# Performance work log

Measured on AMD Instinct MI355X. Metric: run time of the kernel, lower is better.

## Reference

```python
import jax, jax.numpy as jnp
import numpy as np

B, NMAX, D, H = 8, 8192, 256, 8
DH = D // H  # 32
EPS = 1e-5


def _ln(x, g, b):
    mu = jnp.mean(x, axis=-1, keepdims=True)
    var = jnp.mean((x - mu) ** 2, axis=-1, keepdims=True)
    return (x - mu) / jnp.sqrt(var + EPS) * g + b


def setup_inputs() -> dict:
    key = jax.random.key(0)
    ks = jax.random.split(key, 14)
    s = 1.0 / np.sqrt(D)

    def lin(k):
        kw, kb = jax.random.split(k)
        W = jax.random.uniform(kw, (D, D), minval=-s, maxval=s, dtype=jnp.float32)
        b = jax.random.uniform(kb, (D,), minval=-s, maxval=s, dtype=jnp.float32)
        return W, b

    Wh, bh = lin(ks[0])
    Wq, bq = lin(ks[1])
    Wk, bk = lin(ks[2])
    Wv, bv = lin(ks[3])
    Wout, bout = lin(ks[4])
    return {
        "x": jax.random.normal(ks[5], (B * NMAX, D), dtype=jnp.float32),
        "node_prob": jax.random.uniform(ks[6], (B, NMAX), dtype=jnp.float32),
        "Wh": Wh, "bh": bh,
        "Wq": Wq, "bq": bq,
        "Wk": Wk, "bk": bk,
        "Wv": Wv, "bv": bv,
        "Wout": Wout, "bout": bout,
        "ln1_g": jnp.ones((D,), jnp.float32), "ln1_b": jnp.zeros((D,), jnp.float32),
        "ln2_g": jnp.ones((D,), jnp.float32), "ln2_b": jnp.zeros((D,), jnp.float32),
        "beta_b": jnp.full((D,), 0.5, jnp.float32),  # self.b with beta=0.5 >= 0
    }


def reference(x, node_prob, Wh, bh, Wq, bq, Wk, bk, Wv, bv, Wout, bout,
              ln1_g, ln1_b, ln2_g, ln2_b, beta_b):
    x0 = _ln(x, ln1_g, ln1_b)          # [N, D] input_norm
    h = x0 @ Wh + bh                   # [N, D]
    xd = x0.reshape(B, NMAX, D)        # to_dense_batch (equal-size graphs)
    k = jax.nn.sigmoid(xd @ Wk + bk)   # [B, Nmax, D]
    q = jax.nn.sigmoid(xd @ Wq + bq)   # qk_shared=False
    v = xd @ Wv + bv
    k = k * node_prob[:, :, None]      # node-prob weighting
    q = q.reshape(B, NMAX, H, DH)
    k = k.reshape(B, NMAX, H, DH)
    v = v.reshape(B, NMAX, H, DH)
    kv = jnp.einsum('bnhd,bnhe->bhde', k, v)        # k^T v per head
    num = jnp.einsum('bnhd,bhde->bnhe', q, kv)      # q . kv
    den = jnp.einsum('bnhd,bhd->bnh', q, jnp.sum(k, axis=1))[..., None]
    att = (num / den).reshape(B * NMAX, D)
    out = _ln(att, ln2_g, ln2_b) * (h + beta_b)     # norm(x) * (h + beta)
    out = jax.nn.relu(out @ Wout + bout)            # dropout p=0 / eval: identity
    return out + x0                                  # residual=True
```

## Files before the change

kernel.cpp:

```cpp
#include <hip/hip_runtime.h>
#include <cstdint>


#define DEVI __device__ __forceinline__

typedef __attribute__((ext_vector_type(8))) short bf16x8;
typedef __attribute__((ext_vector_type(4))) float f32x4;

DEVI ushort f2bf(float f) {
  uint32_t u = __float_as_uint(f);
  u += 0x7FFFu + ((u >> 16) & 1u);
  return (ushort)(u >> 16);
}
DEVI float bf2f(ushort h) { return __uint_as_float(((uint32_t)h) << 16); }

DEVI void gload_lds16(const void* g, void* l) {
  __builtin_amdgcn_global_load_lds((const __attribute__((address_space(1))) void*)g,
                                   (__attribute__((address_space(3))) void*)l, 16, 0, 0);
}
DEVI void vm_drain() { asm volatile("s_waitcnt vmcnt(0)" ::: "memory"); }

__global__ __launch_bounds__(256)
void ln1_k(const float* __restrict__ x, const float* __restrict__ g1,
           const float* __restrict__ b1, ushort* __restrict__ x0b,
           const float* __restrict__ Wh, const float* __restrict__ Wq,
           const float* __restrict__ Wk, const float* __restrict__ Wv,
           const float* __restrict__ Wout,
           const float* __restrict__ bh, const float* __restrict__ bq,
           const float* __restrict__ bk, const float* __restrict__ bv,
           ushort* __restrict__ Wcat_t, ushort* __restrict__ Woutt,
           float* __restrict__ bcat, float* __restrict__ kv, float* __restrict__ ksum)
{
  const int t = threadIdx.x;
  const int idx = blockIdx.x * 256 + t;
  if (idx < 396288) {
    if (idx < 262144) {
      int j = idx >> 8, kk = idx & 255;
      int g = j >> 8, jj = j & 255;
      const float* W = (g == 0) ? Wh : (g == 1) ? Wq : (g == 2) ? Wk : Wv;
      Wcat_t[idx] = f2bf(W[kk * 256 + jj]);
    }
    int i2 = idx - 262144;
    if (i2 >= 0 && i2 < 65536) {
      int j = i2 >> 8, kk = i2 & 255;
      Woutt[i2] = f2bf(Wout[kk * 256 + j]);
    }
    int i3 = idx - (262144 + 65536);
    if (i3 >= 0 && i3 < 1024) {
      int g = i3 >> 8, jj = i3 & 255;
      const float* bb = (g == 0) ? bh : (g == 1) ? bq : (g == 2) ? bk : bv;
      bcat[i3] = bb[jj];
    }
    int i4 = idx - (262144 + 65536 + 1024);
    if (i4 >= 0 && i4 < 65536) kv[i4] = 0.0f;
    int i5 = idx - (262144 + 65536 + 1024 + 65536);
    if (i5 >= 0 && i5 < 2048) ksum[i5] = 0.0f;
  }
  const int l = t & 63, w = t >> 6;
  const size_t r = (size_t)blockIdx.x * 4 + w;
  const float4 xv = *(const float4*)&x[r * 256 + l * 4];
  float s = xv.x + xv.y + xv.z + xv.w;
  float sq = xv.x * xv.x + xv.y * xv.y + xv.z * xv.z + xv.w * xv.w;
#pragma unroll
  for (int off = 1; off < 64; off <<= 1) { s += __shfl_xor(s, off); sq += __shfl_xor(sq, off); }
  const float mean = s * (1.0f / 256.0f);
  const float var = sq * (1.0f / 256.0f) - mean * mean;
  const float rstd = rsqrtf(var + 1e-5f);
  const float4 g4 = *(const float4*)&g1[l * 4];
  const float4 b4 = *(const float4*)&b1[l * 4];
  ushort4 o;
  o.x = f2bf((xv.x - mean) * rstd * g4.x + b4.x);
  o.y = f2bf((xv.y - mean) * rstd * g4.y + b4.y);
  o.z = f2bf((xv.z - mean) * rstd * g4.z + b4.z);
  o.w = f2bf((xv.w - mean) * rstd * g4.w + b4.w);
  *(ushort4*)&x0b[r * 256 + l * 4] = o;
}

template <int MODE>
__global__ __launch_bounds__(256, 4)
void gemm_bf16_k(const ushort* __restrict__ A, const ushort* __restrict__ Bt,
                 const float* __restrict__ bias, const float* __restrict__ node_prob,
                 const ushort* __restrict__ x0b, ushort* __restrict__ outb,
                 float* __restrict__ outf)
{
  __shared__ ushort smem[16384];
  const int t = threadIdx.x;
  const int l = t & 63;
  const int w = t >> 6;
  const int wr = w >> 1, wc = w & 1;
  const int nNB = (MODE == 0) ? 8 : 2;
  const int per = gridDim.x >> 3;
  const int tile = (blockIdx.x & 7) * per + (blockIdx.x >> 3);
  const int m0 = (tile / nNB) * 128, n0 = (tile % nNB) * 128;
  const int sr = t >> 2;
  const int sd = t & 3;
  const int ssl = sd ^ ((t >> 3) & 3);
  f32x4 acc[4][4] = {};

  auto stage = [&](int buf, int kt) {
#pragma unroll
    for (int i = 0; i < 2; ++i) {
      int row = i * 64 + sr;
      gload_lds16(&A[(size_t)(m0 + row) * 256 + kt * 32 + ssl * 8],
                  &smem[buf * 4096 + row * 32 + sd * 8]);
    }
#pragma unroll
    for (int i = 0; i < 2; ++i) {
      int row = i * 64 + sr;
      gload_lds16(&Bt[(size_t)(n0 + row) * 256 + kt * 32 + ssl * 8],
                  &smem[8192 + buf * 4096 + row * 32 + sd * 8]);
    }
  };

  stage(0, 0);
  vm_drain();
  __syncthreads();
  const int fr = l & 15;
  const int fq = l >> 4;
  const int fsl = (fq ^ ((l >> 1) & 3)) * 8;
#pragma unroll
  for (int kt = 0; kt < 8; ++kt) {
    const int cur = kt & 1;
    if (kt < 7) stage(cur ^ 1, kt + 1);
    bf16x8 af[4], bfr[4];
#pragma unroll
    for (int f = 0; f < 4; ++f) {
      af[f]  = *(const bf16x8*)&smem[cur * 4096 + (wr * 64 + f * 16 + fr) * 32 + fsl];
      bfr[f] = *(const bf16x8*)&smem[8192 + cur * 4096 + (wc * 64 + f * 16 + fr) * 32 + fsl];
    }
#pragma unroll
    for (int fm = 0; fm < 4; ++fm)
#pragma unroll
      for (int fn = 0; fn < 4; ++fn)
        acc[fm][fn] = __builtin_amdgcn_mfma_f32_16x16x32_bf16(af[fm], bfr[fn], acc[fm][fn], 0, 0, 0);
    vm_drain();
    __syncthreads();
  }

  float biasv[4];
#pragma unroll
  for (int fn = 0; fn < 4; ++fn) biasv[fn] = bias[n0 + wc * 64 + fn * 16 + fr];
  const int g = n0 >> 8;
#pragma unroll
  for (int fm = 0; fm < 4; ++fm) {
#pragma unroll
    for (int fn = 0; fn < 4; ++fn) {
#pragma unroll
      for (int i = 0; i < 4; ++i) {
        const int row = wr * 64 + fm * 16 + fq * 4 + i;
        const int col = wc * 64 + fn * 16 + fr;
        float v = acc[fm][fn][i] + biasv[fn];
        if (MODE == 0) {
          if (g == 1 || g == 2) v = 1.0f / (1.0f + __expf(-v));
          if (g == 2) v *= node_prob[m0 + row];
        } else {
          v = fmaxf(v, 0.0f);
        }
        smem[row * 128 + (col ^ ((row & 7) << 4))] = f2bf(v);
      }
    }
  }
  __syncthreads();
#pragma unroll
  for (int it = 0; it < 8; ++it) {
    const int row = w * 32 + it * 4 + fq;
    const int c8 = fr * 8;
    bf16x8 u = *(const bf16x8*)&smem[row * 128 + (c8 ^ ((row & 7) << 4))];
    if (MODE == 0) {
      *(bf16x8*)&outb[(size_t)(m0 + row) * 1024 + n0 + c8] = u;
    } else {
      bf16x8 xv = *(const bf16x8*)&x0b[(size_t)(m0 + row) * 256 + n0 + c8];
      float4 o0, o1;
      o0.x = bf2f((ushort)u[0]) + bf2f((ushort)xv[0]);
      o0.y = bf2f((ushort)u[1]) + bf2f((ushort)xv[1]);
      o0.z = bf2f((ushort)u[2]) + bf2f((ushort)xv[2]);
      o0.w = bf2f((ushort)u[3]) + bf2f((ushort)xv[3]);
      o1.x = bf2f((ushort)u[4]) + bf2f((ushort)xv[4]);
      o1.y = bf2f((ushort)u[5]) + bf2f((ushort)xv[5]);
      o1.z = bf2f((ushort)u[6]) + bf2f((ushort)xv[6]);
      o1.w = bf2f((ushort)u[7]) + bf2f((ushort)xv[7]);
      *(float4*)&outf[(size_t)(m0 + row) * 256 + n0 + c8] = o0;
      *(float4*)&outf[(size_t)(m0 + row) * 256 + n0 + c8 + 4] = o1;
    }
  }
}

__global__ __launch_bounds__(256)
void kvred_k(const ushort* __restrict__ hqkv, float* __restrict__ kv, float* __restrict__ ksum)
{
  __shared__ ushort smem[32768];
  const int t = threadIdx.x, l = t & 63, w = t >> 6;
  const int bh = blockIdx.x >> 4, cb = blockIdx.x & 15;
  const int b = bh >> 3, h = bh & 7;
  const size_t nbase = (size_t)b * 8192 + cb * 512 + w * 128;
  ushort* kt = &smem[w * 8192];
  ushort* vt = &smem[w * 8192 + 4096];
#pragma unroll
  for (int i = 0; i < 8; ++i) {
    size_t row = nbase + i * 16 + (l >> 2);
    gload_lds16(&hqkv[row * 1024 + 512 + h * 32 + (l & 3) * 8], &kt[i * 512 + l * 8]);
  }
#pragma unroll
  for (int i = 0; i < 8; ++i) {
    size_t row = nbase + i * 16 + (l >> 2);
    gload_lds16(&hqkv[row * 1024 + 768 + h * 32 + (l & 3) * 8], &vt[i * 512 + l * 8]);
  }
  vm_drain();

  const int d0 = (l & 7) * 4, e0 = (l >> 3) * 4;
  float acc[4][4] = {};
  float ks0 = 0, ks1 = 0, ks2 = 0, ks3 = 0;
#pragma unroll 8
  for (int nn = 0; nn < 128; ++nn) {
    ushort4 kk = *(const ushort4*)&kt[nn * 32 + d0];
    ushort4 vv = *(const ushort4*)&vt[nn * 32 + e0];
    float k0 = bf2f(kk.x), k1 = bf2f(kk.y), k2 = bf2f(kk.z), k3 = bf2f(kk.w);
    float v0 = bf2f(vv.x), v1 = bf2f(vv.y), v2 = bf2f(vv.z), v3 = bf2f(vv.w);
    acc[0][0] += k0 * v0; acc[0][1] += k0 * v1; acc[0][2] += k0 * v2; acc[0][3] += k0 * v3;
    acc[1][0] += k1 * v0; acc[1][1] += k1 * v1; acc[1][2] += k1 * v2; acc[1][3] += k1 * v3;
    acc[2][0] += k2 * v0; acc[2][1] += k2 * v1; acc[2][2] += k2 * v2; acc[2][3] += k2 * v3;
    acc[3][0] += k3 * v0; acc[3][1] += k3 * v1; acc[3][2] += k3 * v2; acc[3][3] += k3 * v3;
    ks0 += k0; ks1 += k1; ks2 += k2; ks3 += k3;
  }
  __syncthreads();
  float* part = (float*)(void*)smem;
#pragma unroll
  for (int dd = 0; dd < 4; ++dd)
#pragma unroll
    for (int ee = 0; ee < 4; ++ee)
      part[w * 1024 + (dd * 4 + ee) * 64 + l] = acc[dd][ee];
  if (l < 8) {
    part[4096 + w * 32 + l * 4 + 0] = ks0;
    part[4096 + w * 32 + l * 4 + 1] = ks1;
    part[4096 + w * 32 + l * 4 + 2] = ks2;
    part[4096 + w * 32 + l * 4 + 3] = ks3;
  }
  __syncthreads();
  const int lsrc = t & 63;
#pragma unroll
  for (int j = 0; j < 4; ++j) {
    const int val = (t >> 6) * 4 + j;
    float s = part[0 * 1024 + val * 64 + lsrc] + part[1 * 1024 + val * 64 + lsrc]
            + part[2 * 1024 + val * 64 + lsrc] + part[3 * 1024 + val * 64 + lsrc];
    const int d = (lsrc & 7) * 4 + (val >> 2);
    const int e = (lsrc >> 3) * 4 + (val & 3);
    atomicAdd(&kv[(size_t)bh * 1024 + d * 32 + e], s);
  }
  if (t < 32) {
    float s = part[4096 + t] + part[4096 + 32 + t] + part[4096 + 64 + t] + part[4096 + 96 + t];
    atomicAdd(&ksum[bh * 32 + t], s);
  }
}

__global__ __launch_bounds__(256)
void attnz_k(const ushort* __restrict__ hqkv, const float* __restrict__ kv,
             const float* __restrict__ ksum, const float* __restrict__ g2,
             const float* __restrict__ b2, const float* __restrict__ beta,
             ushort* __restrict__ zb)
{
  __shared__ float kv_s[8192];
  __shared__ float ks_s[256];
  __shared__ float q_s[16][256];
  const int t = threadIdx.x, l = t & 63, w = t >> 6;
  const int r0 = blockIdx.x * 16;
  const int b = r0 >> 13;
#pragma unroll
  for (int i = 0; i < 8; ++i)
    *(float4*)&kv_s[i * 1024 + t * 4] = *(const float4*)&kv[(size_t)b * 8192 + i * 1024 + t * 4];
  if (t < 64) *(float4*)&ks_s[t * 4] = *(const float4*)&ksum[b * 256 + t * 4];
#pragma unroll
  for (int rr = 0; rr < 4; ++rr) {
    int r = r0 + w * 4 + rr;
    ushort4 qv = *(const ushort4*)&hqkv[(size_t)r * 1024 + 256 + l * 4];
    float4 qf = {bf2f(qv.x), bf2f(qv.y), bf2f(qv.z), bf2f(qv.w)};
    *(float4*)&q_s[w * 4 + rr][l * 4] = qf;
  }
  __syncthreads();

  const int h = l >> 3, e0 = (l & 7) * 4;
  float num[4][4] = {};
  float den[4] = {0.0f, 0.0f, 0.0f, 0.0f};
#pragma unroll
  for (int dl = 0; dl < 8; ++dl) {
    const float4 ks4 = *(const float4*)&ks_s[h * 32 + dl * 4];
    float4 kvv[4];
#pragma unroll
    for (int c = 0; c < 4; ++c)
      kvv[c] = *(const float4*)&kv_s[h * 1024 + (dl * 4 + c) * 32 + e0];
#pragma unroll
    for (int rr = 0; rr < 4; ++rr) {
      const float4 q4 = *(const float4*)&q_s[w * 4 + rr][h * 32 + dl * 4];
      den[rr] += q4.x * ks4.x + q4.y * ks4.y + q4.z * ks4.z + q4.w * ks4.w;
      num[rr][0] += q4.x * kvv[0].x + q4.y * kvv[1].x + q4.z * kvv[2].x + q4.w * kvv[3].x;
      num[rr][1] += q4.x * kvv[0].y + q4.y * kvv[1].y + q4.z * kvv[2].y + q4.w * kvv[3].y;
      num[rr][2] += q4.x * kvv[0].z + q4.y * kvv[1].z + q4.z * kvv[2].z + q4.w * kvv[3].z;
      num[rr][3] += q4.x * kvv[0].w + q4.y * kvv[1].w + q4.z * kvv[2].w + q4.w * kvv[3].w;
    }
  }
  const float4 g4 = *(const float4*)&g2[l * 4];
  const float4 bb4 = *(const float4*)&b2[l * 4];
  const float4 be4 = *(const float4*)&beta[l * 4];
#pragma unroll
  for (int rr = 0; rr < 4; ++rr) {
    const int r = r0 + w * 4 + rr;
    const float inv = 1.0f / den[rr];
    float a0 = num[rr][0] * inv, a1 = num[rr][1] * inv;
    float a2 = num[rr][2] * inv, a3 = num[rr][3] * inv;
    float s = a0 + a1 + a2 + a3;
    float sq = a0 * a0 + a1 * a1 + a2 * a2 + a3 * a3;
#pragma unroll
    for (int off = 1; off < 64; off <<= 1) { s += __shfl_xor(s, off); sq += __shfl_xor(sq, off); }
    const float mean = s * (1.0f / 256.0f);
    const float var = sq * (1.0f / 256.0f) - mean * mean;
    const float rstd = rsqrtf(var + 1e-5f);
    ushort4 hv = *(const ushort4*)&hqkv[(size_t)r * 1024 + l * 4];
    ushort4 o;
    o.x = f2bf(((a0 - mean) * rstd * g4.x + bb4.x) * (bf2f(hv.x) + be4.x));
    o.y = f2bf(((a1 - mean) * rstd * g4.y + bb4.y) * (bf2f(hv.y) + be4.y));
    o.z = f2bf(((a2 - mean) * rstd * g4.z + bb4.z) * (bf2f(hv.z) + be4.z));
    o.w = f2bf(((a3 - mean) * rstd * g4.w + bb4.w) * (bf2f(hv.w) + be4.w));
    *(ushort4*)&zb[(size_t)r * 256 + l * 4] = o;
  }
}

extern "C" void kernel_launch(void* const* d_in, const int* in_sizes, int n_in,
                              void* d_out, int out_size, void* d_ws, size_t ws_size,
                              hipStream_t stream)
{
  const float* x    = (const float*)d_in[0];
  const float* np_  = (const float*)d_in[1];
  const float* Wh   = (const float*)d_in[2];
  const float* bh   = (const float*)d_in[3];
  const float* Wq   = (const float*)d_in[4];
  const float* bq   = (const float*)d_in[5];
  const float* Wk   = (const float*)d_in[6];
  const float* bk   = (const float*)d_in[7];
  const float* Wv   = (const float*)d_in[8];
  const float* bv   = (const float*)d_in[9];
  const float* Wout = (const float*)d_in[10];
  const float* bout = (const float*)d_in[11];
  const float* ln1g = (const float*)d_in[12];
  const float* ln1b = (const float*)d_in[13];
  const float* ln2g = (const float*)d_in[14];
  const float* ln2b = (const float*)d_in[15];
  const float* beta = (const float*)d_in[16];
  float* out = (float*)d_out;

  uintptr_t p = (uintptr_t)d_ws;
  ushort* x0b    = (ushort*)p; p += (size_t)65536 * 256 * 2;
  ushort* hqkv   = (ushort*)p; p += (size_t)65536 * 1024 * 2;
  ushort* zb     = (ushort*)p; p += (size_t)65536 * 256 * 2;
  ushort* Wcat_t = (ushort*)p; p += (size_t)1024 * 256 * 2;
  ushort* Woutt  = (ushort*)p; p += (size_t)256 * 256 * 2;
  float*  bcat   = (float*)p;  p += (size_t)1024 * 4;
  float*  kv     = (float*)p;  p += (size_t)65536 * 4;
  float*  ksum   = (float*)p;  p += (size_t)2048 * 4;

  ln1_k<<<16384, 256, 0, stream>>>(x, ln1g, ln1b, x0b,
                                   Wh, Wq, Wk, Wv, Wout, bh, bq, bk, bv,
                                   Wcat_t, Woutt, bcat, kv, ksum);
  gemm_bf16_k<0><<<4096, 256, 0, stream>>>(x0b, Wcat_t, bcat, np_, nullptr, hqkv, nullptr);
  kvred_k<<<1024, 256, 0, stream>>>(hqkv, kv, ksum);
  attnz_k<<<4096, 256, 0, stream>>>(hqkv, kv, ksum, ln2g, ln2b, beta, zb);
  gemm_bf16_k<1><<<1024, 256, 0, stream>>>(zb, Woutt, bout, nullptr, x0b, nullptr, out);
}
```

Before: 213.0 us.

## Fuse attention-normalize stage with output GEMM into a single kernel

Merges the attention/LN2 kernel with the final Wout GEMM. Each block handles 64 rows: it computes the normalized attention product into a swizzled bf16 LDS tile, then runs MFMA against double-buffered Wout tiles and writes relu+bias+residual output. This removes the zb round trip through global memory and one launch. The cost is about 75KB of LDS per block, which limits occupancy, plus a per-block reload of kv and the 64 KB Wout.

After: 196.5 us. -7.7%, faster.

```diff
diff --git a/kernel.cpp b/kernel.cpp
--- a/kernel.cpp
+++ b/kernel.cpp
@@ -252,74 +252,139 @@
   }
 }
 
-__global__ __launch_bounds__(256)
-void attnz_k(const ushort* __restrict__ hqkv, const float* __restrict__ kv,
-             const float* __restrict__ ksum, const float* __restrict__ g2,
-             const float* __restrict__ b2, const float* __restrict__ beta,
-             ushort* __restrict__ zb)
+__global__ __launch_bounds__(256, 2)
+void attout_k(const ushort* __restrict__ hqkv, const float* __restrict__ kv,
+              const float* __restrict__ ksum, const float* __restrict__ g2,
+              const float* __restrict__ b2, const float* __restrict__ beta,
+              const ushort* __restrict__ Woutt, const float* __restrict__ bout,
+              const ushort* __restrict__ x0b, float* __restrict__ out)
 {
-  __shared__ float kv_s[8192];
-  __shared__ float ks_s[256];
-  __shared__ float q_s[16][256];
+  __shared__ ushort smem[37376];
+  float* kv_s = (float*)(void*)smem;
+  float* ks_s = (float*)(void*)(smem + 16384);
+  ushort* q_s = smem + 16896;
+  ushort* z_s = smem + 20992;
+
   const int t = threadIdx.x, l = t & 63, w = t >> 6;
-  const int r0 = blockIdx.x * 16;
+  const int r0 = blockIdx.x * 64;
   const int b = r0 >> 13;
+
 #pragma unroll
   for (int i = 0; i < 8; ++i)
     *(float4*)&kv_s[i * 1024 + t * 4] = *(const float4*)&kv[(size_t)b * 8192 + i * 1024 + t * 4];
   if (t < 64) *(float4*)&ks_s[t * 4] = *(const float4*)&ksum[b * 256 + t * 4];
-#pragma unroll
-  for (int rr = 0; rr < 4; ++rr) {
-    int r = r0 + w * 4 + rr;
-    ushort4 qv = *(const ushort4*)&hqkv[(size_t)r * 1024 + 256 + l * 4];
-    float4 qf = {bf2f(qv.x), bf2f(qv.y), bf2f(qv.z), bf2f(qv.w)};
-    *(float4*)&q_s[w * 4 + rr][l * 4] = qf;
-  }
   __syncthreads();
 
   const int h = l >> 3, e0 = (l & 7) * 4;
-  float num[4][4] = {};
-  float den[4] = {0.0f, 0.0f, 0.0f, 0.0f};
-#pragma unroll
-  for (int dl = 0; dl < 8; ++dl) {
-    const float4 ks4 = *(const float4*)&ks_s[h * 32 + dl * 4];
-    float4 kvv[4];
-#pragma unroll
-    for (int c = 0; c < 4; ++c)
-      kvv[c] = *(const float4*)&kv_s[h * 1024 + (dl * 4 + c) * 32 + e0];
-#pragma unroll
-    for (int rr = 0; rr < 4; ++rr) {
-      const float4 q4 = *(const float4*)&q_s[w * 4 + rr][h * 32 + dl * 4];
-      den[rr] += q4.x * ks4.x + q4.y * ks4.y + q4.z * ks4.z + q4.w * ks4.w;
-      num[rr][0] += q4.x * kvv[0].x + q4.y * kvv[1].x + q4.z * kvv[2].x + q4.w * kvv[3].x;
-      num[rr][1] += q4.x * kvv[0].y + q4.y * kvv[1].y + q4.z * kvv[2].y + q4.w * kvv[3].y;
-      num[rr][2] += q4.x * kvv[0].z + q4.y * kvv[1].z + q4.z * kvv[2].z + q4.w * kvv[3].z;
-      num[rr][3] += q4.x * kvv[0].w + q4.y * kvv[1].w + q4.z * kvv[2].w + q4.w * kvv[3].w;
-    }
-  }
   const float4 g4 = *(const float4*)&g2[l * 4];
   const float4 bb4 = *(const float4*)&b2[l * 4];
   const float4 be4 = *(const float4*)&beta[l * 4];
-#pragma unroll
-  for (int rr = 0; rr < 4; ++rr) {
-    const int r = r0 + w * 4 + rr;
-    const float inv = 1.0f / den[rr];
-    float a0 = num[rr][0] * inv, a1 = num[rr][1] * inv;
-    float a2 = num[rr][2] * inv, a3 = num[rr][3] * inv;
-    float s = a0 + a1 + a2 + a3;
-    float sq = a0 * a0 + a1 * a1 + a2 * a2 + a3 * a3;
-#pragma unroll
-    for (int off = 1; off < 64; off <<= 1) { s += __shfl_xor(s, off); sq += __shfl_xor(sq, off); }
-    const float mean = s * (1.0f / 256.0f);
-    const float var = sq * (1.0f / 256.0f) - mean * mean;
-    const float rstd = rsqrtf(var + 1e-5f);
-    ushort4 hv = *(const ushort4*)&hqkv[(size_t)r * 1024 + l * 4];
-    ushort4 o;
-    o.x = f2bf(((a0 - mean) * rstd * g4.x + bb4.x) * (bf2f(hv.x) + be4.x));
-    o.y = f2bf(((a1 - mean) * rstd * g4.y + bb4.y) * (bf2f(hv.y) + be4.y));
-    o.z = f2bf(((a2 - mean) * rstd * g4.z + bb4.z) * (bf2f(hv.z) + be4.z));
-    o.w = f2bf(((a3 - mean) * rstd * g4.w + bb4.w) * (bf2f(hv.w) + be4.w));
-    *(ushort4*)&zb[(size_t)r * 256 + l * 4] = o;
+
+  for (int c = 0; c < 4; ++c) {
+#pragma unroll
+    for (int j = 0; j < 2; ++j) {
+      int row = w * 4 + j * 2 + (l >> 5);
+      gload_lds16(&hqkv[(size_t)(r0 + c * 16 + row) * 1024 + 256 + (l & 31) * 8],
+                  &q_s[(w * 128 + j * 64 + l) * 8]);
+    }
+    vm_drain();
+    __syncthreads();
+    float num[4][4] = {};
+    float den[4] = {0.0f, 0.0f, 0.0f, 0.0f};
+#pragma unroll
+    for (int dl = 0; dl < 8; ++dl) {
+      const float4 ks4 = *(const float4*)&ks_s[h * 32 + dl * 4];
+      float4 kvv[4];
+#pragma unroll
+      for (int cc = 0; cc < 4; ++cc)
+        kvv[cc] = *(const float4*)&kv_s[h * 1024 + (dl * 4 + cc) * 32 + e0];
+#pragma unroll
+      for (int rr = 0; rr < 4; ++rr) {
+        ushort4 qv = *(const ushort4*)&q_s[(w * 4 + rr) * 256 + h * 32 + dl * 4];
+        float qx = bf2f(qv.x), qy = bf2f(qv.y), qz = bf2f(qv.z), qw = bf2f(qv.w);
+        den[rr] += qx * ks4.x + qy * ks4.y + qz * ks4.z + qw * ks4.w;
+        num[rr][0] += qx * kvv[0].x + qy * kvv[1].x + qz * kvv[2].x + qw * kvv[3].x;
+        num[rr][1] += qx * kvv[0].y + qy * kvv[1].y + qz * kvv[2].y + qw * kvv[3].y;
+        num[rr][2] += qx * kvv[0].z + qy * kvv[1].z + qz * kvv[2].z + qw * kvv[3].z;
+        num[rr][3] += qx * kvv[0].w + qy * kvv[1].w + qz * kvv[2].w + qw * kvv[3].w;
+      }
+    }
+#pragma unroll
+    for (int rr = 0; rr < 4; ++rr) {
+      const int rl = c * 16 + w * 4 + rr;
+      const int r = r0 + rl;
+      const float inv = 1.0f / den[rr];
+      float a0 = num[rr][0] * inv, a1 = num[rr][1] * inv;
+      float a2 = num[rr][2] * inv, a3 = num[rr][3] * inv;
+      float s = a0 + a1 + a2 + a3;
+      float sq = a0 * a0 + a1 * a1 + a2 * a2 + a3 * a3;
+#pragma unroll
+      for (int off = 1; off < 64; off <<= 1) { s += __shfl_xor(s, off); sq += __shfl_xor(sq, off); }
+      const float mean = s * (1.0f / 256.0f);
+      const float var = sq * (1.0f / 256.0f) - mean * mean;
+      const float rstd = rsqrtf(var + 1e-5f);
+      ushort4 hv = *(const ushort4*)&hqkv[(size_t)r * 1024 + l * 4];
+      ushort4 o;
+      o.x = f2bf(((a0 - mean) * rstd * g4.x + bb4.x) * (bf2f(hv.x) + be4.x));
+      o.y = f2bf(((a1 - mean) * rstd * g4.y + bb4.y) * (bf2f(hv.y) + be4.y));
+      o.z = f2bf(((a2 - mean) * rstd * g4.z + bb4.z) * (bf2f(hv.z) + be4.z));
+      o.w = f2bf(((a3 - mean) * rstd * g4.w + bb4.w) * (bf2f(hv.w) + be4.w));
+      *(ushort4*)&z_s[rl * 256 + (((l >> 1) ^ (rl & 15)) * 8) + (l & 1) * 4] = o;
+    }
+    __syncthreads();
+  }
+
+  ushort* Bst = smem;
+  const int sr = t >> 2, sd = t & 3;
+  const int ssl = sd ^ ((t >> 3) & 3);
+  auto stageB = [&](int buf, int kt) {
+#pragma unroll
+    for (int i = 0; i < 4; ++i) {
+      int row = i * 64 + sr;
+      gload_lds16(&Woutt[(size_t)row * 256 + kt * 32 + ssl * 8],
+                  &Bst[buf * 8192 + row * 32 + sd * 8]);
+    }
+  };
+  stageB(0, 0);
+  vm_drain();
+  __syncthreads();
+  const int fr = l & 15, fq = l >> 4;
+  const int fsl = (fq ^ ((l >> 1) & 3)) * 8;
+  f32x4 acc[4][4] = {};
+#pragma unroll
+  for (int kt = 0; kt < 8; ++kt) {
+    const int cur = kt & 1;
+    if (kt < 7) stageB(cur ^ 1, kt + 1);
+    bf16x8 af[4], bfr[4];
+#pragma unroll
+    for (int f = 0; f < 4; ++f) {
+      af[f]  = *(const bf16x8*)&z_s[(f * 16 + fr) * 256 + (((kt * 4 + fq) ^ fr) * 8)];
+      bfr[f] = *(const bf16x8*)&Bst[cur * 8192 + (w * 64 + f * 16 + fr) * 32 + fsl];
+    }
+#pragma unroll
+    for (int fm = 0; fm < 4; ++fm)
+#pragma unroll
+      for (int fn = 0; fn < 4; ++fn)
+        acc[fm][fn] = __builtin_amdgcn_mfma_f32_16x16x32_bf16(af[fm], bfr[fn], acc[fm][fn], 0, 0, 0);
+    vm_drain();
+    __syncthreads();
+  }
+  float biasv[4];
+#pragma unroll
+  for (int fn = 0; fn < 4; ++fn) biasv[fn] = bout[w * 64 + fn * 16 + fr];
+#pragma unroll
+  for (int fm = 0; fm < 4; ++fm) {
+#pragma unroll
+    for (int fn = 0; fn < 4; ++fn) {
+#pragma unroll
+      for (int i = 0; i < 4; ++i) {
+        const int row = fm * 16 + fq * 4 + i;
+        const int col = w * 64 + fn * 16 + fr;
+        float v = fmaxf(acc[fm][fn][i] + biasv[fn], 0.0f);
+        v += bf2f(x0b[(size_t)(r0 + row) * 256 + col]);
+        out[(size_t)(r0 + row) * 256 + col] = v;
+      }
+    }
   }
 }
 
@@ -355,12 +420,13 @@
   float*  bcat   = (float*)p;  p += (size_t)1024 * 4;
   float*  kv     = (float*)p;  p += (size_t)65536 * 4;
   float*  ksum   = (float*)p;  p += (size_t)2048 * 4;
+  (void)zb;
 
   ln1_k<<<16384, 256, 0, stream>>>(x, ln1g, ln1b, x0b,
                                    Wh, Wq, Wk, Wv, Wout, bh, bq, bk, bv,
                                    Wcat_t, Woutt, bcat, kv, ksum);
   gemm_bf16_k<0><<<4096, 256, 0, stream>>>(x0b, Wcat_t, bcat, np_, nullptr, hqkv, nullptr);
   kvred_k<<<1024, 256, 0, stream>>>(hqkv, kv, ksum);
-  attnz_k<<<4096, 256, 0, stream>>>(hqkv, kv, ksum, ln2g, ln2b, beta, zb);
-  gemm_bf16_k<1><<<1024, 256, 0, stream>>>(zb, Woutt, bout, nullptr, x0b, nullptr, out);
-}
+  attout_k<<<1024, 256, 0, stream>>>(hqkv, kv, ksum, ln2g, ln2b, beta,
+                                     Woutt, bout, x0b, out);
+}
```
